# Kernel optimization log

Measured on AMD Instinct MI355X. Metric: run time of the kernel, lower is better.

Reference implementation:

```python
import jax, jax.numpy as jnp
import numpy as np

N = 100000   # nodes
E = 300000   # edges
D_IN = 128   # input feature dim
H = 256      # hidden dim
L = 4        # GIN layers
G = 512      # graphs in batch
BN_EPS = 1e-5


def setup_inputs() -> dict:
    key = jax.random.key(0)
    ks = jax.random.split(key, 12)
    s = 0.02
    return {
        "x": jax.random.normal(ks[0], (N, D_IN), jnp.float32),
        "edge_index": jax.random.randint(ks[1], (2, E), 0, N, dtype=jnp.int32),
        "batch": jnp.sort(jax.random.randint(ks[2], (N,), 0, G, dtype=jnp.int32)),
        "W_in": jax.random.normal(ks[3], (D_IN, H), jnp.float32) * s,
        "b_in": jnp.zeros((H,), jnp.float32),
        "eps": jnp.zeros((L,), jnp.float32),           # GINConv train_eps init = 0
        "W1": jax.random.normal(ks[4], (L, H, 2 * H), jnp.float32) * s,
        "b1": jnp.zeros((L, 2 * H), jnp.float32),
        "W2": jax.random.normal(ks[5], (L, 2 * H, H), jnp.float32) * s,
        "b2": jnp.zeros((L, H), jnp.float32),
        "gamma": jnp.ones((L, H), jnp.float32),
        "beta": jnp.zeros((L, H), jnp.float32),
        "Wp1": jax.random.normal(ks[6], (H, H // 2), jnp.float32) * s,
        "bp1": jnp.zeros((H // 2,), jnp.float32),
        "Wp2": jax.random.normal(ks[7], (H // 2, 1), jnp.float32) * s,
        "bp2": jnp.zeros((1,), jnp.float32),
    }


def reference(x, edge_index, batch, W_in, b_in, eps, W1, b1, W2, b2,
              gamma, beta, Wp1, bp1, Wp2, bp2):
    src, dst = edge_index[0], edge_index[1]

    # input projection + relu
    h = jax.nn.relu(x @ W_in + b_in)  # [N, H]

    def layer(h, p):
        e, w1, bb1, w2, bb2, g, bt = p
        # GINConv: sum-aggregate neighbor messages at destination nodes
        agg = jax.ops.segment_sum(h[src], dst, num_segments=N)  # [N, H]
        z = (1.0 + e) * h + agg
        # GIN MLP: H -> 2H -> H
        z = jax.nn.relu(z @ w1 + bb1) @ w2 + bb2
        # BatchNorm over node dim (training-mode batch statistics, biased var)
        mu = jnp.mean(z, axis=0)
        var = jnp.var(z, axis=0)
        z = g * (z - mu) * jax.lax.rsqrt(var + BN_EPS) + bt
        return jax.nn.relu(z), None

    h, _ = jax.lax.scan(layer, h, (eps, W1, b1, W2, b2, gamma, beta))

    # global mean pool per graph
    sums = jax.ops.segment_sum(h, batch, num_segments=G)                       # [G, H]
    counts = jax.ops.segment_sum(jnp.ones((N, 1), h.dtype), batch, num_segments=G)
    pooled = sums / jnp.maximum(counts, 1.0)

    # predictor head (dropout is identity in eval)
    out = jax.nn.relu(pooled @ Wp1 + bp1) @ Wp2 + bp2  # [G, 1]
    return out
```

## Files before the change

kernel.cpp:

```cpp
#include <hip/hip_runtime.h>

#define NN 100000
#define NP 100096
#define EE 300000
#define DIN 128
#define HD  256
#define HD2 512
#define NL  4
#define NG  512
#define BN_EPS 1e-5f

typedef __attribute__((ext_vector_type(8))) short s8v;
typedef __attribute__((ext_vector_type(4))) float f4v;

typedef unsigned short ushort_t;

static __device__ inline ushort_t f2bf(float f) {
    unsigned u = __float_as_uint(f);
    unsigned r = (u + 0x7fffu + ((u >> 16) & 1u)) >> 16;
    return (ushort_t)r;
}
static __device__ inline float bf2f(ushort_t h) {
    return __uint_as_float(((unsigned)h) << 16);
}
static __device__ inline float blo(unsigned v) { return __uint_as_float(v << 16); }
static __device__ inline float bhi(unsigned v) { return __uint_as_float(v & 0xffff0000u); }

static __device__ inline void gacc(float* A, const uint4 u,
                                   const float4 s0, const float4 s1,
                                   const float4 h0, const float4 h1, float wg) {
    A[0] += wg * fmaxf(blo(u.x) * s0.x + h0.x, 0.f);
    A[1] += wg * fmaxf(bhi(u.x) * s0.y + h0.y, 0.f);
    A[2] += wg * fmaxf(blo(u.y) * s0.z + h0.z, 0.f);
    A[3] += wg * fmaxf(bhi(u.y) * s0.w + h0.w, 0.f);
    A[4] += wg * fmaxf(blo(u.z) * s1.x + h1.x, 0.f);
    A[5] += wg * fmaxf(bhi(u.z) * s1.y + h1.y, 0.f);
    A[6] += wg * fmaxf(blo(u.w) * s1.z + h1.z, 0.f);
    A[7] += wg * fmaxf(bhi(u.w) * s1.w + h1.w, 0.f);
}

#define GLOAD_LDS16(g, l) __builtin_amdgcn_global_load_lds( \
    (const __attribute__((address_space(1))) unsigned int*)(const void*)(g), \
    (__attribute__((address_space(3))) unsigned int*)(void*)(l), 16, 0, 0)

#define WAITCNT_VM8 0xF78
#define WAITCNT_VM4 0xF74
#define WAITCNT_VM0 0xF70

__global__ __launch_bounds__(256) void pack_w1_kernel(
    const float* __restrict__ W1, ushort_t* __restrict__ W1P)
{
    const int t = threadIdx.x, L = t & 63;
    const int gu = blockIdx.x * 4 + (t >> 6);
    const int l = gu >> 8, rem = gu & 255;
    const int c = rem >> 4, u = rem & 15;
    const int kk = u >> 1, nt = u & 1;
    const int h  = c * 32 + nt * 16 + (L & 15);
    const int k0 = kk * 32 + (L >> 4) * 8;
    const float* src = W1 + (size_t)l * HD * HD2;
    s8v v;
#pragma unroll
    for (int e = 0; e < 8; ++e)
        v[e] = (short)f2bf(src[(size_t)(k0 + e) * HD2 + h]);
    *(s8v*)(W1P + (size_t)gu * 512 + L * 8) = v;
}

__global__ __launch_bounds__(256) void pack_w2_kernel(
    const float* __restrict__ W2, ushort_t* __restrict__ W2P)
{
    const int t = threadIdx.x, L = t & 63;
    const int gu = blockIdx.x * 4 + (t >> 6);
    const int l = gu >> 8, rem = gu & 255;
    const int c = rem >> 4, nt = rem & 15;
    const int h  = nt * 16 + (L & 15);
    const int k0 = c * 32 + (L >> 4) * 8;
    const float* src = W2 + (size_t)l * HD2 * HD;
    s8v v;
#pragma unroll
    for (int e = 0; e < 8; ++e)
        v[e] = (short)f2bf(src[(size_t)(k0 + e) * HD + h]);
    *(s8v*)(W2P + (size_t)gu * 512 + L * 8) = v;
}

__global__ __launch_bounds__(256) void pack_win_kernel(
    const float* __restrict__ Win, ushort_t* __restrict__ WinP)
{
    const int t = threadIdx.x, L = t & 63;
    const int gu = blockIdx.x * 4 + (t >> 6);
    const int kk = gu >> 4, nt = gu & 15;
    const int h  = nt * 16 + (L & 15);
    const int k0 = kk * 32 + (L >> 4) * 8;
    s8v v;
#pragma unroll
    for (int e = 0; e < 8; ++e)
        v[e] = (short)f2bf(Win[(size_t)(k0 + e) * HD + h]);
    *(s8v*)(WinP + (size_t)gu * 512 + L * 8) = v;
}

__global__ __launch_bounds__(512, 2) void inproj_kernel(
    const float* __restrict__ x,
    const ushort_t* __restrict__ WinP,
    const float* __restrict__ bias,
    ushort_t* __restrict__ C)
{
    extern __shared__ char smem[];
    ushort_t* Ws = (ushort_t*)smem;
    const int tid = threadIdx.x;
    const int w   = tid >> 6;
    const int L   = tid & 63;
    const int lm  = L & 15;
    const int q   = L >> 4;
    const int row0 = blockIdx.x * 128;

#pragma unroll
    for (int i = 0; i < 8; ++i) {
        const int u = w * 8 + i;
        GLOAD_LDS16(WinP + u * 512 + L * 8, Ws + u * 512);
    }

    const int row = row0 + w * 16 + lm;
    const float* xr = x + (size_t)min(row, NN - 1) * DIN;
    s8v a[4];
#pragma unroll
    for (int kk = 0; kk < 4; ++kk) {
        const float4 u0 = *(const float4*)(xr + kk * 32 + q * 8);
        const float4 u1 = *(const float4*)(xr + kk * 32 + q * 8 + 4);
        s8v v;
        v[0] = (short)f2bf(u0.x); v[1] = (short)f2bf(u0.y);
        v[2] = (short)f2bf(u0.z); v[3] = (short)f2bf(u0.w);
        v[4] = (short)f2bf(u1.x); v[5] = (short)f2bf(u1.y);
        v[6] = (short)f2bf(u1.z); v[7] = (short)f2bf(u1.w);
        a[kk] = v;
    }
    __builtin_amdgcn_s_waitcnt(WAITCNT_VM0);
    __syncthreads();

    f4v acc[16] = {};
#pragma unroll
    for (int kk = 0; kk < 4; ++kk) {
#pragma unroll
        for (int nt = 0; nt < 16; ++nt) {
            s8v b = *(const s8v*)&Ws[(kk * 16 + nt) * 512 + L * 8];
            acc[nt] = __builtin_amdgcn_mfma_f32_16x16x32_bf16(a[kk], b, acc[nt], 0, 0, 0);
        }
    }
    __syncthreads();

    ushort_t* Cs = Ws;
#pragma unroll
    for (int nt = 0; nt < 16; ++nt) {
        const float bj = bias[nt * 16 + lm];
#pragma unroll
        for (int r = 0; r < 4; ++r) {
            const int rr = w * 16 + q * 4 + r;
            Cs[rr * 256 + nt * 16 + lm] = f2bf(fmaxf(acc[nt][r] + bj, 0.f));
        }
    }
    __syncthreads();
#pragma unroll
    for (int i = 0; i < 8; ++i) {
        const int idx = i * 512 + tid;
        const int rr = idx >> 5, ch = idx & 31;
        const s8v v = *(const s8v*)&Cs[idx * 8];
        *(s8v*)(C + (size_t)(row0 + rr) * HD + ch * 8) = v;
    }
}

__global__ __launch_bounds__(512, 4) void fused_mlp_kernel(
    const ushort_t* __restrict__ A,
    const ushort_t* __restrict__ W1l,
    const float*    __restrict__ b1l,
    const ushort_t* __restrict__ W2l,
    const float*    __restrict__ b2l,
    ushort_t* __restrict__ C,
    float* __restrict__ stats)
{
    extern __shared__ char smem[];
    ushort_t* lds = (ushort_t*)smem;
    const int tid = threadIdx.x;
    const int w   = tid >> 6;
    const int L   = tid & 63;
    const int lm  = L & 15;
    const int q   = L >> 4;
    const int row0 = blockIdx.x * 128;

    float* b1s = (float*)(smem + 75776);
    char*  hcb = smem + 65536 + w * 1280;

    if (tid < HD2) b1s[tid] = b1l[tid];
    __syncthreads();

    const ushort_t* Arow = A + (size_t)(row0 + w * 16 + lm) * HD;
    s8v a[8];
#pragma unroll
    for (int kk = 0; kk < 8; ++kk)
        a[kk] = *(const s8v*)(Arow + kk * 32 + q * 8);
    __builtin_amdgcn_s_waitcnt(WAITCNT_VM0);

#define STAGE_W(buf, cc) do {                                                 \
    ushort_t* Wb_ = lds + (buf) * 16384;                                      \
    if (w < 4) {                                                              \
        _Pragma("unroll")                                                     \
        for (int i_ = 0; i_ < 4; ++i_) {                                      \
            const int u_ = w * 4 + i_;                                        \
            GLOAD_LDS16(W1l + ((cc) * 16 + u_) * 512 + L * 8,                 \
                        Wb_ + u_ * 512);                                      \
        }                                                                     \
    } else {                                                                  \
        _Pragma("unroll")                                                     \
        for (int i_ = 0; i_ < 4; ++i_) {                                      \
            const int u_ = (w - 4) * 4 + i_;                                  \
            GLOAD_LDS16(W2l + ((cc) * 16 + u_) * 512 + L * 8,                 \
                        Wb_ + 8192 + u_ * 512);                               \
        }                                                                     \
    }                                                                         \
} while (0)

    STAGE_W(0, 0);
    STAGE_W(1, 1);

    f4v acc2[16] = {};
    for (int c = 0; c < 16; ++c) {
        if (c < 15) __builtin_amdgcn_s_waitcnt(WAITCNT_VM4);
        else        __builtin_amdgcn_s_waitcnt(WAITCNT_VM0);
        __builtin_amdgcn_s_barrier();
        __builtin_amdgcn_sched_barrier(0);

        const ushort_t* Wb  = lds + (c & 1) * 16384;
        const ushort_t* W2b = Wb + 8192;

        f4v acc1[2] = {};
        __builtin_amdgcn_s_setprio(1);
#pragma unroll
        for (int kk = 0; kk < 8; ++kk) {
#pragma unroll
            for (int nt = 0; nt < 2; ++nt) {
                s8v b = *(const s8v*)&Wb[(kk * 2 + nt) * 512 + L * 8];
                acc1[nt] = __builtin_amdgcn_mfma_f32_16x16x32_bf16(a[kk], b, acc1[nt], 0, 0, 0);
            }
        }
        __builtin_amdgcn_s_setprio(0);

#pragma unroll
        for (int nt = 0; nt < 2; ++nt) {
            const float bj = b1s[c * 32 + nt * 16 + lm];
#pragma unroll
            for (int r = 0; r < 4; ++r) {
                const int rr = q * 4 + r;
                *(ushort_t*)(hcb + rr * 80 + (nt * 16 + lm) * 2) =
                    f2bf(fmaxf(acc1[nt][r] + bj, 0.f));
            }
        }
        const s8v at = *(const s8v*)(hcb + lm * 80 + q * 16);
        __builtin_amdgcn_s_setprio(1);
#pragma unroll
        for (int nt = 0; nt < 16; ++nt) {
            s8v b = *(const s8v*)&W2b[nt * 512 + L * 8];
            acc2[nt] = __builtin_amdgcn_mfma_f32_16x16x32_bf16(at, b, acc2[nt], 0, 0, 0);
        }
        __builtin_amdgcn_s_setprio(0);

        __builtin_amdgcn_sched_barrier(0);
        __builtin_amdgcn_s_barrier();
        if (c + 2 < 16) STAGE_W((c & 1), c + 2);
    }
#undef STAGE_W

    __syncthreads();

    ushort_t* Cs = lds;
    float* ssum  = (float*)(smem + 65536);
    float* ssq   = (float*)(smem + 73728);

#pragma unroll
    for (int nt = 0; nt < 16; ++nt) {
        const float bj = b2l[nt * 16 + lm];
        float s = 0.f, sq = 0.f;
#pragma unroll
        for (int r = 0; r < 4; ++r) {
            const float f  = acc2[nt][r] + bj;
            const int row  = w * 16 + q * 4 + r;
            Cs[row * 256 + nt * 16 + lm] = f2bf(f);
            if (row0 + row < NN) { s += f; sq += f * f; }
        }
        s  += __shfl_xor(s, 16, 64);  s  += __shfl_xor(s, 32, 64);
        sq += __shfl_xor(sq, 16, 64); sq += __shfl_xor(sq, 32, 64);
        if (q == 0) {
            ssum[w * 256 + nt * 16 + lm] = s;
            ssq [w * 256 + nt * 16 + lm] = sq;
        }
    }
    __syncthreads();

#pragma unroll
    for (int i = 0; i < 8; ++i) {
        const int idx = i * 512 + tid;
        const int row = idx >> 5, ch = idx & 31;
        const s8v v = *(const s8v*)&Cs[idx * 8];
        *(s8v*)(C + (size_t)(row0 + row) * HD + ch * 8) = v;
    }
    if (tid < HD) {
        float s = 0.f, sq = 0.f;
#pragma unroll
        for (int ww = 0; ww < 8; ++ww) {
            s  += ssum[ww * 256 + tid];
            sq += ssq [ww * 256 + tid];
        }
        unsafeAtomicAdd(&stats[tid], s);
        unsafeAtomicAdd(&stats[HD + tid], sq);
    }
}

__global__ __launch_bounds__(256) void zero_kernel(float* __restrict__ p, long n4)
{
    const long i = (long)blockIdx.x * 256 + threadIdx.x;
    if (i < n4) ((float4*)p)[i] = make_float4(0.f, 0.f, 0.f, 0.f);
}

__global__ __launch_bounds__(256) void init_stats_kernel(float* __restrict__ stats)
{
    const int t = threadIdx.x;
#pragma unroll
    for (int i = 0; i < 2 * NL; ++i) stats[i * HD + t] = 0.f;
}

__global__ __launch_bounds__(256) void hist_kernel(
    const int* __restrict__ dst, int* __restrict__ deg, int E)
{
    const int e = blockIdx.x * 256 + threadIdx.x;
    if (e < E) atomicAdd(&deg[dst[e]], 1);
}

__global__ __launch_bounds__(256) void scan1_kernel(
    const int* __restrict__ deg, int* __restrict__ partial,
    int* __restrict__ bsums, int n)
{
    __shared__ int tmp[256];
    const int i = blockIdx.x * 256 + threadIdx.x;
    const int v = (i < n) ? deg[i] : 0;
    tmp[threadIdx.x] = v;
    __syncthreads();
    for (int off = 1; off < 256; off <<= 1) {
        const int t = (threadIdx.x >= off) ? tmp[threadIdx.x - off] : 0;
        __syncthreads();
        tmp[threadIdx.x] += t;
        __syncthreads();
    }
    if (i < n) partial[i] = tmp[threadIdx.x] - v;
    if (threadIdx.x == 255) bsums[blockIdx.x] = tmp[255];
}

__global__ __launch_bounds__(512) void scan2_kernel(int* __restrict__ bsums, int nb)
{
    __shared__ int tmp[512];
    const int i = threadIdx.x;
    const int v = (i < nb) ? bsums[i] : 0;
    tmp[i] = v;
    __syncthreads();
    for (int off = 1; off < 512; off <<= 1) {
        const int t = (i >= off) ? tmp[i - off] : 0;
        __syncthreads();
        tmp[i] += t;
        __syncthreads();
    }
    if (i < nb) bsums[i] = tmp[i] - v;
}

__global__ __launch_bounds__(256) void scan3_kernel(
    const int* __restrict__ partial, const int* __restrict__ bsums,
    int* __restrict__ offs, int* __restrict__ cursor, int n)
{
    const int i = blockIdx.x * 256 + threadIdx.x;
    if (i < n) {
        const int o = partial[i] + bsums[blockIdx.x];
        offs[i] = o;
        cursor[i] = o;
    }
}

__global__ __launch_bounds__(256) void scatter_kernel(
    const int* __restrict__ src, const int* __restrict__ dst,
    int* __restrict__ cursor, int* __restrict__ srcSorted, int E)
{
    const int e = blockIdx.x * 256 + threadIdx.x;
    if (e >= E) return;
    const int p = atomicAdd(&cursor[dst[e]], 1);
    srcSorted[p] = src[e];
}

__global__ __launch_bounds__(256) void aggregate_kernel(
    const ushort_t* __restrict__ z, const int* __restrict__ offs,
    const int* __restrict__ deg, const int* __restrict__ srcSorted,
    const float* __restrict__ epsArr, int epsIdx,
    const float* __restrict__ statsPrev,
    const float* __restrict__ gammaPrev, const float* __restrict__ betaPrev,
    ushort_t* __restrict__ out)
{
    __shared__ float ssc[HD];
    __shared__ float ssh[HD];
    const int t = threadIdx.x;
    {
        float sc = 1.f, sh = 0.f;
        if (statsPrev) {
            const float invN = 1.0f / (float)NN;
            const float mu  = statsPrev[t] * invN;
            const float var = statsPrev[HD + t] * invN - mu * mu;
            const float inv = rsqrtf(var + BN_EPS);
            sc = gammaPrev[t] * inv;
            sh = betaPrev[t] - mu * sc;
        }
        ssc[t] = sc;
        ssh[t] = sh;
    }
    __syncthreads();

    const int n = blockIdx.x * 8 + (t >> 5);
    const int L = t & 31;
    const int c0 = L * 8;
    const float4 scA = *(const float4*)(ssc + c0);
    const float4 scB = *(const float4*)(ssc + c0 + 4);
    const float4 shA = *(const float4*)(ssh + c0);
    const float4 shB = *(const float4*)(ssh + c0 + 4);
    const int start = offs[n];
    const int dc = deg[n];
    float a[8] = {};
    float b[8] = {};
    int j = 0;
    for (; j + 1 < dc; j += 2) {
        const int s0 = srcSorted[start + j];
        const int s1 = srcSorted[start + j + 1];
        const uint4 u = *(const uint4*)(z + (size_t)s0 * HD + c0);
        const uint4 v = *(const uint4*)(z + (size_t)s1 * HD + c0);
        gacc(a, u, scA, scB, shA, shB, 1.f);
        gacc(b, v, scA, scB, shA, shB, 1.f);
    }
    if (j < dc) {
        const int s0 = srcSorted[start + j];
        const uint4 u = *(const uint4*)(z + (size_t)s0 * HD + c0);
        gacc(a, u, scA, scB, shA, shB, 1.f);
    }
#pragma unroll
    for (int k = 0; k < 8; ++k) a[k] += b[k];

    const float se = 1.0f + epsArr[epsIdx];
    const uint4 hs = *(const uint4*)(z + (size_t)n * HD + c0);
    gacc(a, hs, scA, scB, shA, shB, se);

    uint4 o;
    o.x = (unsigned)f2bf(a[0]) | ((unsigned)f2bf(a[1]) << 16);
    o.y = (unsigned)f2bf(a[2]) | ((unsigned)f2bf(a[3]) << 16);
    o.z = (unsigned)f2bf(a[4]) | ((unsigned)f2bf(a[5]) << 16);
    o.w = (unsigned)f2bf(a[6]) | ((unsigned)f2bf(a[7]) << 16);
    *(uint4*)(out + (size_t)n * HD + c0) = o;
}

__global__ __launch_bounds__(256) void pool_head_kernel(
    const ushort_t* __restrict__ z, const int* __restrict__ batch,
    const float* __restrict__ statsPrev,
    const float* __restrict__ gammaPrev, const float* __restrict__ betaPrev,
    const float* __restrict__ Wp1, const float* __restrict__ bp1,
    const float* __restrict__ Wp2, const float* __restrict__ bp2,
    float* __restrict__ out)
{
    __shared__ float ssc[HD];
    __shared__ float ssh[HD];
    __shared__ float poolw[4][HD];
    __shared__ float pool[HD];
    __shared__ float red[128];
    __shared__ int seg[2];
    const int g = blockIdx.x;
    const int t = threadIdx.x;
    const int w = t >> 6;
    const int L = t & 63;
    {
        const float invN = 1.0f / (float)NN;
        const float mu  = statsPrev[t] * invN;
        const float var = statsPrev[HD + t] * invN - mu * mu;
        const float inv = rsqrtf(var + BN_EPS);
        const float sc  = gammaPrev[t] * inv;
        ssc[t] = sc;
        ssh[t] = betaPrev[t] - mu * sc;
    }
    if (t == 0) {
        int lo = 0, hi = NN;
        while (lo < hi) { const int m = (lo + hi) >> 1; if (batch[m] < g) lo = m + 1; else hi = m; }
        seg[0] = lo;
        hi = NN;
        while (lo < hi) { const int m = (lo + hi) >> 1; if (batch[m] < g + 1) lo = m + 1; else hi = m; }
        seg[1] = lo;
    }
    __syncthreads();
    const int start = seg[0], end = seg[1];
    const int c0 = L * 4;
    const float4 sc = *(const float4*)(ssc + c0);
    const float4 sh = *(const float4*)(ssh + c0);
    float a0 = 0.f, a1 = 0.f, a2 = 0.f, a3 = 0.f;
    float b0 = 0.f, b1 = 0.f, b2 = 0.f, b3 = 0.f;
    int r = start + w;
    for (; r + 4 < end; r += 8) {
        const ushort4 u = *(const ushort4*)(z + (size_t)r * HD + c0);
        const ushort4 v = *(const ushort4*)(z + (size_t)(r + 4) * HD + c0);
        a0 += fmaxf(bf2f(u.x) * sc.x + sh.x, 0.f);
        a1 += fmaxf(bf2f(u.y) * sc.y + sh.y, 0.f);
        a2 += fmaxf(bf2f(u.z) * sc.z + sh.z, 0.f);
        a3 += fmaxf(bf2f(u.w) * sc.w + sh.w, 0.f);
        b0 += fmaxf(bf2f(v.x) * sc.x + sh.x, 0.f);
        b1 += fmaxf(bf2f(v.y) * sc.y + sh.y, 0.f);
        b2 += fmaxf(bf2f(v.z) * sc.z + sh.z, 0.f);
        b3 += fmaxf(bf2f(v.w) * sc.w + sh.w, 0.f);
    }
    if (r < end) {
        const ushort4 u = *(const ushort4*)(z + (size_t)r * HD + c0);
        a0 += fmaxf(bf2f(u.x) * sc.x + sh.x, 0.f);
        a1 += fmaxf(bf2f(u.y) * sc.y + sh.y, 0.f);
        a2 += fmaxf(bf2f(u.z) * sc.z + sh.z, 0.f);
        a3 += fmaxf(bf2f(u.w) * sc.w + sh.w, 0.f);
    }
    poolw[w][c0 + 0] = a0 + b0;
    poolw[w][c0 + 1] = a1 + b1;
    poolw[w][c0 + 2] = a2 + b2;
    poolw[w][c0 + 3] = a3 + b3;
    __syncthreads();
    const float invC = 1.0f / (float)max(end - start, 1);
    pool[t] = (poolw[0][t] + poolw[1][t] + poolw[2][t] + poolw[3][t]) * invC;
    __syncthreads();
    if (t < 128) {
        float acc = 0.f;
#pragma unroll 4
        for (int k = 0; k < HD; ++k)
            acc += pool[k] * Wp1[k * 128 + t];
        red[t] = fmaxf(acc + bp1[t], 0.f) * Wp2[t];
    }
    __syncthreads();
    for (int sft = 64; sft > 0; sft >>= 1) {
        if (t < sft) red[t] += red[t + sft];
        __syncthreads();
    }
    if (t == 0) out[g] = red[0] + bp2[0];
}

extern "C" void kernel_launch(void* const* d_in, const int* in_sizes, int n_in,
                              void* d_out, int out_size, void* d_ws, size_t ws_size,
                              hipStream_t stream)
{
    const float* x     = (const float*)d_in[0];
    const int*   ei    = (const int*)  d_in[1];
    const int*   batch = (const int*)  d_in[2];
    const float* W_in  = (const float*)d_in[3];
    const float* b_in  = (const float*)d_in[4];
    const float* eps   = (const float*)d_in[5];
    const float* W1    = (const float*)d_in[6];
    const float* b1    = (const float*)d_in[7];
    const float* W2    = (const float*)d_in[8];
    const float* b2    = (const float*)d_in[9];
    const float* gamma = (const float*)d_in[10];
    const float* beta  = (const float*)d_in[11];
    const float* Wp1   = (const float*)d_in[12];
    const float* bp1   = (const float*)d_in[13];
    const float* Wp2   = (const float*)d_in[14];
    const float* bp2   = (const float*)d_in[15];

    const int* srcIdx = ei;
    const int* dstIdx = ei + EE;

    char* p = (char*)d_ws;
    ushort_t* zbuf    = (ushort_t*)p;  p += (size_t)NP * HD  * 2;
    ushort_t* abuf    = (ushort_t*)p;  p += (size_t)NP * HD  * 2;
    ushort_t* W1P     = (ushort_t*)p;  p += (size_t)NL * HD2 * HD * 2;
    ushort_t* W2P     = (ushort_t*)p;  p += (size_t)NL * HD * HD2 * 2;
    ushort_t* WinP    = (ushort_t*)p;  p += (size_t)HD * DIN * 2;
    int* deg          = (int*)p;       p += (size_t)NN * 4;
    int* partial      = (int*)p;       p += (size_t)NN * 4;
    int* bsums        = (int*)p;       p += 512 * 4;
    int* offs         = (int*)p;       p += (size_t)NN * 4;
    int* cursor       = (int*)p;       p += (size_t)NN * 4;
    int* srcSorted    = (int*)p;       p += (size_t)EE * 4;
    float* stats      = (float*)p;     p += (size_t)NL * 2 * HD * 4;

    const int nb = (NN + 255) / 256;
    const int INPROJ_LDS = 65536;
    const int FUSED_LDS  = 81920;

    init_stats_kernel<<<1, 256, 0, stream>>>(stats);

    pack_win_kernel<<<16, 256, 0, stream>>>(W_in, WinP);
    pack_w1_kernel<<<256, 256, 0, stream>>>(W1, W1P);
    pack_w2_kernel<<<256, 256, 0, stream>>>(W2, W2P);

    zero_kernel<<<(NN / 4 + 255) / 256, 256, 0, stream>>>((float*)deg, NN / 4);
    hist_kernel<<<(EE + 255) / 256, 256, 0, stream>>>(dstIdx, deg, EE);
    scan1_kernel<<<nb, 256, 0, stream>>>(deg, partial, bsums, NN);
    scan2_kernel<<<1, 512, 0, stream>>>(bsums, nb);
    scan3_kernel<<<nb, 256, 0, stream>>>(partial, bsums, offs, cursor, NN);
    scatter_kernel<<<(EE + 255) / 256, 256, 0, stream>>>(srcIdx, dstIdx, cursor, srcSorted, EE);

    inproj_kernel<<<NP / 128, 512, INPROJ_LDS, stream>>>(x, WinP, b_in, zbuf);

    for (int l = 0; l < NL; ++l) {
        const float* sp = (l == 0) ? nullptr : stats + (size_t)(l - 1) * 2 * HD;
        const int gl = (l == 0) ? 0 : l - 1;
        aggregate_kernel<<<NN / 8, 256, 0, stream>>>(
            zbuf, offs, deg, srcSorted, eps, l,
            sp, gamma + (size_t)gl * HD, beta + (size_t)gl * HD, abuf);

        fused_mlp_kernel<<<NP / 128, 512, FUSED_LDS, stream>>>(
            abuf, W1P + (size_t)l * HD2 * HD, b1 + (size_t)l * HD2,
            W2P + (size_t)l * HD * HD2, b2 + (size_t)l * HD, zbuf,
            stats + (size_t)l * 2 * HD);
    }

    pool_head_kernel<<<NG, 256, 0, stream>>>(
        zbuf, batch, stats + (size_t)(NL - 1) * 2 * HD,
        gamma + (size_t)(NL - 1) * HD, beta + (size_t)(NL - 1) * HD,
        Wp1, bp1, Wp2, bp2, (float*)d_out);
}
```

Baseline: 720.9 us.

## Single-buffer weight staging in fused MLP to cut LDS and raise occupancy

Replaces the double-buffered W1/W2 chunk staging in LDS with a single buffer, which drops the fused kernel's shared memory from 80 KB to 52 KB and raises the launch-bounds occupancy hint from 4 to 6. The output write-back goes through LDS in two 64-row passes so it fits in the smaller buffer. The cost is that each chunk's weight load is no longer prefetched: every iteration waits for the full load and adds an extra barrier, exposing global-load latency. The higher occupancy is meant to hide that latency across blocks.

```diff
diff --git a/kernel.cpp b/kernel.cpp
--- a/kernel.cpp
+++ b/kernel.cpp
@@ -166,7 +166,7 @@
     }
 }
 
-__global__ __launch_bounds__(512, 4) void fused_mlp_kernel(
+__global__ __launch_bounds__(512, 6) void fused_mlp_kernel(
     const ushort_t* __restrict__ A,
     const ushort_t* __restrict__ W1l,
     const float*    __restrict__ b1l,
@@ -184,8 +184,8 @@
     const int q   = L >> 4;
     const int row0 = blockIdx.x * 128;
 
-    float* b1s = (float*)(smem + 75776);
-    char*  hcb = smem + 65536 + w * 1280;
+    float* b1s = (float*)(smem + 43008);
+    char*  hcb = smem + 32768 + w * 1280;
 
     if (tid < HD2) b1s[tid] = b1l[tid];
     __syncthreads();
@@ -197,37 +197,33 @@
         a[kk] = *(const s8v*)(Arow + kk * 32 + q * 8);
     __builtin_amdgcn_s_waitcnt(WAITCNT_VM0);
 
-#define STAGE_W(buf, cc) do {                                                 \
-    ushort_t* Wb_ = lds + (buf) * 16384;                                      \
+#define STAGE_W(cc) do {                                                      \
     if (w < 4) {                                                              \
         _Pragma("unroll")                                                     \
         for (int i_ = 0; i_ < 4; ++i_) {                                      \
             const int u_ = w * 4 + i_;                                        \
             GLOAD_LDS16(W1l + ((cc) * 16 + u_) * 512 + L * 8,                 \
-                        Wb_ + u_ * 512);                                      \
+                        lds + u_ * 512);                                      \
         }                                                                     \
     } else {                                                                  \
         _Pragma("unroll")                                                     \
         for (int i_ = 0; i_ < 4; ++i_) {                                      \
             const int u_ = (w - 4) * 4 + i_;                                  \
             GLOAD_LDS16(W2l + ((cc) * 16 + u_) * 512 + L * 8,                 \
-                        Wb_ + 8192 + u_ * 512);                               \
+                        lds + 8192 + u_ * 512);                               \
         }                                                                     \
     }                                                                         \
 } while (0)
 
-    STAGE_W(0, 0);
-    STAGE_W(1, 1);
+    STAGE_W(0);
+    __builtin_amdgcn_s_waitcnt(WAITCNT_VM0);
+    __builtin_amdgcn_s_barrier();
 
     f4v acc2[16] = {};
     for (int c = 0; c < 16; ++c) {
-        if (c < 15) __builtin_amdgcn_s_waitcnt(WAITCNT_VM4);
-        else        __builtin_amdgcn_s_waitcnt(WAITCNT_VM0);
-        __builtin_amdgcn_s_barrier();
         __builtin_amdgcn_sched_barrier(0);
-
-        const ushort_t* Wb  = lds + (c & 1) * 16384;
-        const ushort_t* W2b = Wb + 8192;
+        const ushort_t* Wb  = lds;
+        const ushort_t* W2b = lds + 8192;
 
         f4v acc1[2] = {};
         __builtin_amdgcn_s_setprio(1);
@@ -259,18 +255,22 @@
             acc2[nt] = __builtin_amdgcn_mfma_f32_16x16x32_bf16(at, b, acc2[nt], 0, 0, 0);
         }
         __builtin_amdgcn_s_setprio(0);
-
         __builtin_amdgcn_sched_barrier(0);
+
         __builtin_amdgcn_s_barrier();
-        if (c + 2 < 16) STAGE_W((c & 1), c + 2);
+        if (c < 15) {
+            STAGE_W(c + 1);
+            __builtin_amdgcn_s_waitcnt(WAITCNT_VM0);
+            __builtin_amdgcn_s_barrier();
+        }
     }
 #undef STAGE_W
 
     __syncthreads();
 
     ushort_t* Cs = lds;
-    float* ssum  = (float*)(smem + 65536);
-    float* ssq   = (float*)(smem + 73728);
+    float* ssum  = (float*)(smem + 32768);
+    float* ssq   = (float*)(smem + 40960);
 
 #pragma unroll
     for (int nt = 0; nt < 16; ++nt) {
@@ -278,9 +278,8 @@
         float s = 0.f, sq = 0.f;
 #pragma unroll
         for (int r = 0; r < 4; ++r) {
-            const float f  = acc2[nt][r] + bj;
-            const int row  = w * 16 + q * 4 + r;
-            Cs[row * 256 + nt * 16 + lm] = f2bf(f);
+            const float f = acc2[nt][r] + bj;
+            const int row = w * 16 + q * 4 + r;
             if (row0 + row < NN) { s += f; sq += f * f; }
         }
         s  += __shfl_xor(s, 16, 64);  s  += __shfl_xor(s, 32, 64);
@@ -291,14 +290,6 @@
         }
     }
     __syncthreads();
-
-#pragma unroll
-    for (int i = 0; i < 8; ++i) {
-        const int idx = i * 512 + tid;
-        const int row = idx >> 5, ch = idx & 31;
-        const s8v v = *(const s8v*)&Cs[idx * 8];
-        *(s8v*)(C + (size_t)(row0 + row) * HD + ch * 8) = v;
-    }
     if (tid < HD) {
         float s = 0.f, sq = 0.f;
 #pragma unroll
@@ -308,6 +299,30 @@
         }
         unsafeAtomicAdd(&stats[tid], s);
         unsafeAtomicAdd(&stats[HD + tid], sq);
+    }
+
+#pragma unroll
+    for (int pass = 0; pass < 2; ++pass) {
+        __syncthreads();
+        if ((w >> 2) == pass) {
+#pragma unroll
+            for (int nt = 0; nt < 16; ++nt) {
+                const float bj = b2l[nt * 16 + lm];
+#pragma unroll
+                for (int r = 0; r < 4; ++r) {
+                    const int lrow = (w & 3) * 16 + q * 4 + r;
+                    Cs[lrow * 256 + nt * 16 + lm] = f2bf(acc2[nt][r] + bj);
+                }
+            }
+        }
+        __syncthreads();
+#pragma unroll
+        for (int i = 0; i < 4; ++i) {
+            const int idx = i * 512 + tid;
+            const int lrow = idx >> 5, ch = idx & 31;
+            const s8v v = *(const s8v*)&Cs[idx * 8];
+            *(s8v*)(C + (size_t)(row0 + pass * 64 + lrow) * HD + ch * 8) = v;
+        }
     }
 }
 
@@ -579,7 +594,7 @@
 
     const int nb = (NN + 255) / 256;
     const int INPROJ_LDS = 65536;
-    const int FUSED_LDS  = 81920;
+    const int FUSED_LDS  = 53248;
 
     init_stats_kernel<<<1, 256, 0, stream>>>(stats);
 
```

After: 1.456 ms. 102% more time.
